# Kernel optimization log

Measured on AMD Instinct MI355X. Metric: run time of the kernel, lower is better.

## Reference

```python
import jax, jax.numpy as jnp
import numpy as np

N = 50000
E = 400000
IN_C, HID, OUT2, NCLS = 128, 512, 64, 2
NEG_SLOPE = 0.2


def setup_inputs() -> dict:
    key = jax.random.key(0)
    ks = jax.random.split(key, 12)
    x = jax.random.normal(ks[0], (N, IN_C), dtype=jnp.float32)
    edge_index = jax.random.randint(ks[1], (2, E), 0, N, dtype=jnp.int64)
    def glorot(k, shape):
        fan_in = shape[0]
        return jax.random.normal(k, shape, dtype=jnp.float32) / np.float32(np.sqrt(fan_in))
    return {
        "x": x,
        "edge_index": edge_index,
        "W1": glorot(ks[2], (IN_C, HID)),
        "a1_src": glorot(ks[3], (HID,)),
        "a1_dst": glorot(ks[4], (HID,)),
        "b1": jnp.zeros((HID,), jnp.float32),
        "W2": glorot(ks[5], (HID, OUT2)),
        "a2_src": glorot(ks[6], (OUT2,)),
        "a2_dst": glorot(ks[7], (OUT2,)),
        "b2": jnp.zeros((OUT2,), jnp.float32),
        "fcW": glorot(ks[8], (OUT2, NCLS)),
        "fcb": jnp.zeros((NCLS,), jnp.float32),
    }


def _gat_conv(h_in, src, dst, W, a_src, a_dst, b):
    # single-head GATConv (PyG defaults: heads=1, negative_slope=0.2, self-loops already added)
    h = h_in @ W                                   # [N, D]
    alpha_s = h @ a_src                            # [N]
    alpha_d = h @ a_dst                            # [N]
    e = jax.nn.leaky_relu(alpha_s[src] + alpha_d[dst], NEG_SLOPE)  # [E']
    # segment softmax over incoming edges of each dst node
    m = jax.ops.segment_max(e, dst, num_segments=N)
    ex = jnp.exp(e - m[dst])
    denom = jax.ops.segment_sum(ex, dst, num_segments=N)
    alpha = ex / denom[dst]                        # [E']
    out = jax.ops.segment_sum(alpha[:, None] * h[src], dst, num_segments=N)
    return out + b


def reference(x, edge_index, W1, a1_src, a1_dst, b1, W2, a2_src, a2_dst, b2, fcW, fcb):
    loops = jnp.arange(N, dtype=edge_index.dtype)
    src = jnp.concatenate([edge_index[0], loops])  # add self loops (PyG default)
    dst = jnp.concatenate([edge_index[1], loops])
    h = jax.nn.relu(_gat_conv(x, src, dst, W1, a1_src, a1_dst, b1))
    h = jax.nn.relu(_gat_conv(h, src, dst, W2, a2_src, a2_dst, b2))
    # F.dropout(training=self.training): identity in eval mode
    return h @ fcW + fcb
```

## Files before the change

kernel.cpp:

```cpp
#include <hip/hip_runtime.h>

#define N_NODES 50000
#define N_EDGES 400000
#define E_TOT   (N_EDGES + N_NODES)
#define IN_C 128
#define HID  512
#define OUT2 64
#define NEG_SLOPE 0.2f

typedef short bf16x8 __attribute__((ext_vector_type(8)));
typedef float f32x4  __attribute__((ext_vector_type(4)));

__device__ __forceinline__ float wave_sum(float v) {
#pragma unroll
  for (int o = 32; o > 0; o >>= 1) v += __shfl_xor(v, o, 64);
  return v;
}
__device__ __forceinline__ int wave_sum_i(int v) {
#pragma unroll
  for (int o = 32; o > 0; o >>= 1) v += __shfl_xor(v, o, 64);
  return v;
}
__device__ __forceinline__ float wave_max(float v) {
#pragma unroll
  for (int o = 32; o > 0; o >>= 1) v = fmaxf(v, __shfl_xor(v, o, 64));
  return v;
}
__device__ __forceinline__ float leaky(float t) {
  return (t > 0.f) ? t : NEG_SLOPE * t;
}

__device__ __forceinline__ unsigned short bf16_rne(float x) {
  unsigned u = __float_as_uint(x);
  u += 0x7fffu + ((u >> 16) & 1u);
  return (unsigned short)(u >> 16);
}
__device__ __forceinline__ void split_bf16(float x, unsigned short& h, unsigned short& l) {
  h = bf16_rne(x);
  float hf = __uint_as_float(((unsigned)h) << 16);
  l = bf16_rne(x - hf);
}

__device__ __forceinline__ int esrc(const int* __restrict__ ei, int e) {
  return (e < N_EDGES) ? ei[e] : (e - N_EDGES);
}
__device__ __forceinline__ int edst(const int* __restrict__ ei, int e) {
  return (e < N_EDGES) ? ei[N_EDGES + e] : (e - N_EDGES);
}

__global__ void count_deg(const int* __restrict__ ei, int* __restrict__ deg) {
  int e = blockIdx.x * blockDim.x + threadIdx.x;
  if (e >= E_TOT) return;
  atomicAdd(&deg[edst(ei, e)], 1);
}

__global__ void scanA(const int* __restrict__ deg, int* __restrict__ bsum) {
  __shared__ int ws[16];
  int t = threadIdx.x, lane = t & 63, w = t >> 6;
  int i = blockIdx.x * 1024 + t;
  int v = (i < N_NODES) ? deg[i] : 0;
  int s = wave_sum_i(v);
  if (lane == 0) ws[w] = s;
  __syncthreads();
  if (t == 0) {
    int tot = 0;
#pragma unroll
    for (int k = 0; k < 16; k++) tot += ws[k];
    bsum[blockIdx.x] = tot;
  }
}

__global__ void scanB(const int* __restrict__ bsum, int* __restrict__ boff, int nb) {
  int lane = threadIdx.x;
  int v = (lane < nb) ? bsum[lane] : 0;
  int sc = v;
#pragma unroll
  for (int off = 1; off < 64; off <<= 1) {
    int u = __shfl_up(sc, off, 64);
    if (lane >= off) sc += u;
  }
  if (lane < nb) boff[lane] = sc - v;
}

__global__ void scanC(const int* __restrict__ deg, const int* __restrict__ boff,
                      int* __restrict__ row_ptr) {
  __shared__ int ws[16];
  int t = threadIdx.x, lane = t & 63, w = t >> 6;
  int i = blockIdx.x * 1024 + t;
  int v = (i < N_NODES) ? deg[i] : 0;
  int sc = v;
#pragma unroll
  for (int off = 1; off < 64; off <<= 1) {
    int u = __shfl_up(sc, off, 64);
    if (lane >= off) sc += u;
  }
  if (lane == 63) ws[w] = sc;
  __syncthreads();
  if (w == 0 && lane < 16) {
    int u = ws[lane];
#pragma unroll
    for (int off = 1; off < 16; off <<= 1) {
      int uu = __shfl_up(u, off, 64);
      if (lane >= off) u += uu;
    }
    ws[lane] = u;
  }
  __syncthreads();
  int excl = ((w > 0) ? ws[w - 1] : 0) + boff[blockIdx.x];
  if (i < N_NODES) row_ptr[i + 1] = sc + excl;
  if (blockIdx.x == 0 && t == 0) row_ptr[0] = 0;
}

__global__ void fill_csr(const int* __restrict__ ei, const int* __restrict__ row_ptr,
                         int* __restrict__ cursor, int* __restrict__ csr_src) {
  int e = blockIdx.x * blockDim.x + threadIdx.x;
  if (e >= E_TOT) return;
  int d = edst(ei, e);
  int pos = atomicAdd(&cursor[d], 1);
  csr_src[row_ptr[d] + pos] = esrc(ei, e);
}

__global__ void prep_w1_frag(const float* __restrict__ W1, unsigned short* __restrict__ W1F) {
  int t = blockIdx.x * 256 + threadIdx.x;
  if (t >= 128 * 64) return;
  int fi = t >> 6, l = t & 63;
  int ks = fi & 3, n = (fi >> 2) & 3, jt = fi >> 4;
  int col = jt * 64 + n * 16 + (l & 15);
  int k0 = ks * 32 + (l >> 4) * 8;
  unsigned short hv[8], lv[8];
#pragma unroll
  for (int e = 0; e < 8; e++)
    split_bf16(W1[(size_t)(k0 + e) * HID + col], hv[e], lv[e]);
  unsigned short* ph = W1F + ((size_t)(fi * 2 + 0) * 64 + l) * 8;
  unsigned short* pl = W1F + ((size_t)(fi * 2 + 1) * 64 + l) * 8;
#pragma unroll
  for (int e = 0; e < 8; e++) { ph[e] = hv[e]; pl[e] = lv[e]; }
}

__global__ void prep_w2_frag(const float* __restrict__ W2, unsigned short* __restrict__ W2F) {
  int t = blockIdx.x * 256 + threadIdx.x;
  if (t >= 64 * 64) return;
  int fi = t >> 6, l = t & 63;
  int n = fi & 3, ks = (fi >> 2) & 1, jt = fi >> 3;
  int col = n * 16 + (l & 15);
  int k0 = jt * 64 + ks * 32 + (l >> 4) * 8;
  unsigned short hv[8], lv[8];
#pragma unroll
  for (int e = 0; e < 8; e++)
    split_bf16(W2[(size_t)(k0 + e) * OUT2 + col], hv[e], lv[e]);
  unsigned short* ph = W2F + ((size_t)(fi * 2 + 0) * 64 + l) * 8;
  unsigned short* pl = W2F + ((size_t)(fi * 2 + 1) * 64 + l) * 8;
#pragma unroll
  for (int e = 0; e < 8; e++) { ph[e] = hv[e]; pl[e] = lv[e]; }
}

__global__ void matvec_w1(const float* __restrict__ W1, const float* __restrict__ a1s,
                          const float* __restrict__ a1d, float* __restrict__ w1s,
                          float* __restrict__ w1d) {
  int wid = (blockIdx.x * blockDim.x + threadIdx.x) >> 6;
  int lane = threadIdx.x & 63;
  if (wid >= IN_C) return;
  const float* row = W1 + (size_t)wid * HID;
  float s = 0.f, d = 0.f;
#pragma unroll
  for (int j0 = 0; j0 < HID; j0 += 64) {
    float w = row[j0 + lane];
    s += w * a1s[j0 + lane];
    d += w * a1d[j0 + lane];
  }
  s = wave_sum(s); d = wave_sum(d);
  if (lane == 0) { w1s[wid] = s; w1d[wid] = d; }
}

__global__ void node_scores128(const float* __restrict__ x, const float* __restrict__ ws,
                               const float* __restrict__ wd, float* __restrict__ as_,
                               float* __restrict__ ad_) {
  int wid = (blockIdx.x * blockDim.x + threadIdx.x) >> 6;
  int lane = threadIdx.x & 63;
  if (wid >= N_NODES) return;
  float2 v = ((const float2*)(x + (size_t)wid * IN_C))[lane];
  float2 w1 = ((const float2*)ws)[lane];
  float2 w2 = ((const float2*)wd)[lane];
  float s = wave_sum(v.x * w1.x + v.y * w1.y);
  float d = wave_sum(v.x * w2.x + v.y * w2.y);
  if (lane == 0) { as_[wid] = s; ad_[wid] = d; }
}

__global__ void sm_agg1(const int* __restrict__ row_ptr, const int* __restrict__ csr_src,
                        const float* __restrict__ as_, const float* __restrict__ ad_,
                        const float* __restrict__ x, float* __restrict__ xa) {
  int wid = (blockIdx.x * blockDim.x + threadIdx.x) >> 6;
  int lane = threadIdx.x & 63;
  if (wid >= N_NODES) return;
  int beg = row_ptr[wid], end = row_ptr[wid + 1];
  int deg = end - beg;
  float adv = ad_[wid];
  float2 acc = make_float2(0.f, 0.f);
  if (deg <= 64) {
    int s = 0; float sc = -3.4e38f;
    if (lane < deg) { s = csr_src[beg + lane]; sc = leaky(as_[s] + adv); }
    float m = wave_max(sc);
    float ex = (lane < deg) ? __expf(sc - m) : 0.f;
    float sum = wave_sum(ex);
    float a = ex / sum;
    for (int kk = 0; kk < deg; kk++) {
      float w = __shfl(a, kk, 64);
      int sv = __shfl(s, kk, 64);
      float2 r = ((const float2*)(x + (size_t)sv * IN_C))[lane];
      acc.x += w * r.x; acc.y += w * r.y;
    }
  } else {
    float m = -3.4e38f;
    for (int k = beg + lane; k < end; k += 64)
      m = fmaxf(m, leaky(as_[csr_src[k]] + adv));
    m = wave_max(m);
    float sum = 0.f;
    for (int k = beg + lane; k < end; k += 64)
      sum += __expf(leaky(as_[csr_src[k]] + adv) - m);
    sum = wave_sum(sum);
    float inv = 1.f / sum;
    for (int k = beg; k < end; k++) {
      int sv = csr_src[k];
      float w = __expf(leaky(as_[sv] + adv) - m) * inv;
      float2 r = ((const float2*)(x + (size_t)sv * IN_C))[lane];
      acc.x += w * r.x; acc.y += w * r.y;
    }
  }
  ((float2*)(xa + (size_t)wid * IN_C))[lane] = acc;
}

__launch_bounds__(256, 2)
__global__ void fused_gemm_mfma(const float* __restrict__ xa,
                                const unsigned short* __restrict__ W1F,
                                const float* __restrict__ b1,
                                const unsigned short* __restrict__ W2F,
                                const float* __restrict__ a2s, const float* __restrict__ a2d,
                                float* __restrict__ h2, float* __restrict__ as2,
                                float* __restrict__ ad2) {
  __shared__ unsigned short Ah[64][128];
  __shared__ unsigned short Al[64][128];
  __shared__ unsigned int   TS[64][64];
  int m0 = blockIdx.x * 64;
  int t = threadIdx.x;
  int w = t >> 6;
  int l = t & 63;
  int lr = l & 15;
  int G  = l >> 4;

#pragma unroll
  for (int j = 0; j < 8; j++) {
    int idx = t + j * 256;
    int row = idx >> 5, c4 = idx & 31;
    int gr = m0 + row;
    float4 v = make_float4(0.f, 0.f, 0.f, 0.f);
    if (gr < N_NODES) v = *(const float4*)(xa + (size_t)gr * IN_C + c4 * 4);
    int k0 = (c4 * 4) ^ ((row & 7) << 3);
    unsigned short h0, l0, h1, l1, h2_, l2_, h3, l3;
    split_bf16(v.x, h0, l0); split_bf16(v.y, h1, l1);
    split_bf16(v.z, h2_, l2_); split_bf16(v.w, h3, l3);
    *(uint2*)&Ah[row][k0] = make_uint2((unsigned)h0 | ((unsigned)h1 << 16),
                                       (unsigned)h2_ | ((unsigned)h3 << 16));
    *(uint2*)&Al[row][k0] = make_uint2((unsigned)l0 | ((unsigned)l1 << 16),
                                       (unsigned)l2_ | ((unsigned)l3 << 16));
  }
  __syncthreads();

  int rowA = w * 16 + lr;
  int swA = (rowA & 7) << 3;
  int sw2 = (rowA & 7) << 2;

  bf16x8 aFh[4], aFl[4];
#pragma unroll
  for (int ks = 0; ks < 4; ks++) {
    int kb = (ks * 32 + G * 8) ^ swA;
    aFh[ks] = *(const bf16x8*)&Ah[rowA][kb];
    aFl[ks] = *(const bf16x8*)&Al[rowA][kb];
  }

  const bf16x8* W1Fv = (const bf16x8*)W1F;
  const bf16x8* W2Fv = (const bf16x8*)W2F;

  f32x4 acc2[4];
#pragma unroll
  for (int n = 0; n < 4; n++) acc2[n] = (f32x4){0.f, 0.f, 0.f, 0.f};

  for (int jt = 0; jt < 8; jt++) {
    f32x4 acc1[4];
#pragma unroll
    for (int n = 0; n < 4; n++) acc1[n] = (f32x4){0.f, 0.f, 0.f, 0.f};
#pragma unroll
    for (int ks = 0; ks < 4; ks++) {
#pragma unroll
      for (int n = 0; n < 4; n++) {
        int fi = (jt * 4 + n) * 4 + ks;
        bf16x8 b_h = W1Fv[(size_t)(fi * 2 + 0) * 64 + l];
        bf16x8 b_l = W1Fv[(size_t)(fi * 2 + 1) * 64 + l];
        acc1[n] = __builtin_amdgcn_mfma_f32_16x16x32_bf16(aFh[ks], b_h, acc1[n], 0, 0, 0);
        acc1[n] = __builtin_amdgcn_mfma_f32_16x16x32_bf16(aFl[ks], b_h, acc1[n], 0, 0, 0);
        acc1[n] = __builtin_amdgcn_mfma_f32_16x16x32_bf16(aFh[ks], b_l, acc1[n], 0, 0, 0);
      }
    }
    __syncthreads();
#pragma unroll
    for (int n = 0; n < 4; n++) {
      float bv = b1[jt * 64 + n * 16 + lr];
#pragma unroll
      for (int r = 0; r < 4; r++) {
        float vv = fmaxf(acc1[n][r] + bv, 0.f);
        unsigned short hh, ll;
        split_bf16(vv, hh, ll);
        int rowL = w * 16 + G * 4 + r;
        int colS = (n * 16 + lr) ^ ((rowL & 7) << 2);
        TS[rowL][colS] = (unsigned)hh | ((unsigned)ll << 16);
      }
    }
    __syncthreads();
#pragma unroll
    for (int ks = 0; ks < 2; ks++) {
      int kl = ks * 32 + G * 8;
      uint4 q0 = *(const uint4*)&TS[rowA][(kl + 0) ^ sw2];
      uint4 q1 = *(const uint4*)&TS[rowA][(kl + 4) ^ sw2];
      bf16x8 a2h, a2l;
      a2h[0] = (short)(q0.x & 0xffff); a2l[0] = (short)(q0.x >> 16);
      a2h[1] = (short)(q0.y & 0xffff); a2l[1] = (short)(q0.y >> 16);
      a2h[2] = (short)(q0.z & 0xffff); a2l[2] = (short)(q0.z >> 16);
      a2h[3] = (short)(q0.w & 0xffff); a2l[3] = (short)(q0.w >> 16);
      a2h[4] = (short)(q1.x & 0xffff); a2l[4] = (short)(q1.x >> 16);
      a2h[5] = (short)(q1.y & 0xffff); a2l[5] = (short)(q1.y >> 16);
      a2h[6] = (short)(q1.z & 0xffff); a2l[6] = (short)(q1.z >> 16);
      a2h[7] = (short)(q1.w & 0xffff); a2l[7] = (short)(q1.w >> 16);
#pragma unroll
      for (int n = 0; n < 4; n++) {
        int fi2 = (jt * 2 + ks) * 4 + n;
        bf16x8 b_h = W2Fv[(size_t)(fi2 * 2 + 0) * 64 + l];
        bf16x8 b_l = W2Fv[(size_t)(fi2 * 2 + 1) * 64 + l];
        acc2[n] = __builtin_amdgcn_mfma_f32_16x16x32_bf16(a2h, b_h, acc2[n], 0, 0, 0);
        acc2[n] = __builtin_amdgcn_mfma_f32_16x16x32_bf16(a2l, b_h, acc2[n], 0, 0, 0);
        acc2[n] = __builtin_amdgcn_mfma_f32_16x16x32_bf16(a2h, b_l, acc2[n], 0, 0, 0);
      }
    }
  }

#pragma unroll
  for (int r = 0; r < 4; r++) {
    int grow = m0 + w * 16 + G * 4 + r;
    if (grow < N_NODES) {
#pragma unroll
      for (int n = 0; n < 4; n++)
        h2[(size_t)grow * OUT2 + n * 16 + lr] = acc2[n][r];
    }
    float sp = 0.f, dp = 0.f;
#pragma unroll
    for (int n = 0; n < 4; n++) {
      float v = acc2[n][r];
      sp += v * a2s[n * 16 + lr];
      dp += v * a2d[n * 16 + lr];
    }
#pragma unroll
    for (int o = 1; o < 16; o <<= 1) {
      sp += __shfl_xor(sp, o, 64);
      dp += __shfl_xor(dp, o, 64);
    }
    if (lr == 0 && grow < N_NODES) { as2[grow] = sp; ad2[grow] = dp; }
  }
}

__global__ void sm_agg2_final(const int* __restrict__ row_ptr, const int* __restrict__ csr_src,
                              const float* __restrict__ as_, const float* __restrict__ ad_,
                              const float* __restrict__ h2, const float* __restrict__ b2,
                              const float* __restrict__ fcW, const float* __restrict__ fcb,
                              float* __restrict__ out) {
  int wid = (blockIdx.x * blockDim.x + threadIdx.x) >> 6;
  int lane = threadIdx.x & 63;
  if (wid >= N_NODES) return;
  int beg = row_ptr[wid], end = row_ptr[wid + 1];
  int deg = end - beg;
  float adv = ad_[wid];
  float acc = 0.f;
  if (deg <= 64) {
    int s = 0; float sc = -3.4e38f;
    if (lane < deg) { s = csr_src[beg + lane]; sc = leaky(as_[s] + adv); }
    float m = wave_max(sc);
    float ex = (lane < deg) ? __expf(sc - m) : 0.f;
    float sum = wave_sum(ex);
    float a = ex / sum;
    for (int kk = 0; kk < deg; kk++) {
      float w = __shfl(a, kk, 64);
      int sv = __shfl(s, kk, 64);
      acc += w * h2[(size_t)sv * OUT2 + lane];
    }
  } else {
    float m = -3.4e38f;
    for (int k = beg + lane; k < end; k += 64)
      m = fmaxf(m, leaky(as_[csr_src[k]] + adv));
    m = wave_max(m);
    float sum = 0.f;
    for (int k = beg + lane; k < end; k += 64)
      sum += __expf(leaky(as_[csr_src[k]] + adv) - m);
    sum = wave_sum(sum);
    float inv = 1.f / sum;
    for (int k = beg; k < end; k++) {
      int sv = csr_src[k];
      float w = __expf(leaky(as_[sv] + adv) - m) * inv;
      acc += w * h2[(size_t)sv * OUT2 + lane];
    }
  }
  float v = fmaxf(acc + b2[lane], 0.f);
  float2 fw = ((const float2*)fcW)[lane];
  float f0 = wave_sum(v * fw.x);
  float f1 = wave_sum(v * fw.y);
  if (lane == 0) {
    out[(size_t)wid * 2 + 0] = f0 + fcb[0];
    out[(size_t)wid * 2 + 1] = f1 + fcb[1];
  }
}

extern "C" void kernel_launch(void* const* d_in, const int* in_sizes, int n_in,
                              void* d_out, int out_size, void* d_ws, size_t ws_size,
                              hipStream_t stream) {
  const float* x    = (const float*)d_in[0];
  const int*   ei   = (const int*)d_in[1];
  const float* W1   = (const float*)d_in[2];
  const float* a1s  = (const float*)d_in[3];
  const float* a1d  = (const float*)d_in[4];
  const float* b1   = (const float*)d_in[5];
  const float* W2   = (const float*)d_in[6];
  const float* a2s  = (const float*)d_in[7];
  const float* a2d  = (const float*)d_in[8];
  const float* b2   = (const float*)d_in[9];
  const float* fcW  = (const float*)d_in[10];
  const float* fcb  = (const float*)d_in[11];
  float* out = (float*)d_out;

  char* p = (char*)d_ws;
  float* xa    = (float*)p; p += (size_t)N_NODES * IN_C * 4;
  float* h2    = (float*)p; p += (size_t)N_NODES * OUT2 * 4;
  float* as1   = (float*)p; p += (size_t)N_NODES * 4;
  float* ad1   = (float*)p; p += (size_t)N_NODES * 4;
  float* w1s   = (float*)p; p += 256 * 4;
  float* w1d   = (float*)p; p += 256 * 4;
  int* row_ptr = (int*)p;   p += (size_t)(N_NODES + 4) * 4;
  int* deg     = (int*)p;   p += (size_t)N_NODES * 4;
  int* bsum    = (int*)p;   p += 64 * 4;
  int* boff    = (int*)p;   p += 64 * 4;
  int* csr_src = (int*)p;   p += (size_t)E_TOT * 4;
  unsigned short* W1F = (unsigned short*)p; p += (size_t)128 * 2 * 64 * 8 * 2;
  unsigned short* W2F = (unsigned short*)p; p += (size_t)64 * 2 * 64 * 8 * 2;

  const int edge_blocks = (E_TOT + 255) / 256;
  const int node_wave_blocks = (N_NODES + 3) / 4;
  const int m_tiles = (N_NODES + 63) / 64;
  const int scan_blocks = (N_NODES + 1023) / 1024;

  hipMemsetAsync(deg, 0, (size_t)N_NODES * 4, stream);
  count_deg<<<edge_blocks, 256, 0, stream>>>(ei, deg);
  scanA<<<scan_blocks, 1024, 0, stream>>>(deg, bsum);
  scanB<<<1, 64, 0, stream>>>(bsum, boff, scan_blocks);
  scanC<<<scan_blocks, 1024, 0, stream>>>(deg, boff, row_ptr);
  hipMemsetAsync(deg, 0, (size_t)N_NODES * 4, stream);
  fill_csr<<<edge_blocks, 256, 0, stream>>>(ei, row_ptr, deg, csr_src);
  prep_w1_frag<<<(128 * 64 + 255) / 256, 256, 0, stream>>>(W1, W1F);
  prep_w2_frag<<<(64 * 64 + 255) / 256, 256, 0, stream>>>(W2, W2F);

  matvec_w1<<<(IN_C + 3) / 4, 256, 0, stream>>>(W1, a1s, a1d, w1s, w1d);
  node_scores128<<<node_wave_blocks, 256, 0, stream>>>(x, w1s, w1d, as1, ad1);
  sm_agg1<<<node_wave_blocks, 256, 0, stream>>>(row_ptr, csr_src, as1, ad1, x, xa);

  fused_gemm_mfma<<<m_tiles, 256, 0, stream>>>(xa, W1F, b1, W2F,
                                               a2s, a2d, h2, as1, ad1);

  sm_agg2_final<<<node_wave_blocks, 256, 0, stream>>>(row_ptr, csr_src, as1, ad1, h2, b2,
                                                      fcW, fcb, out);
}
```

Baseline: 308.3 us.

## Give each GEMM wave two row tiles and unroll gather loops by four

The fused MFMA kernel now runs two waves per block, and each wave owns 32 rows (two 16-row M tiles). Each W1/W2 fragment loaded from global memory is therefore reused across twice as many MFMAs. A-fragments are loaded straight from global memory into registers, which removes the Ah/Al shared staging and the block barriers, since each wave only touches its own rows of TS. Both softmax-aggregation kernels unroll the neighbour gather loop by four so several row loads are in flight at once. The cost is higher register pressure in the GEMM and fewer waves per block.

```diff
diff --git a/kernel.cpp b/kernel.cpp
--- a/kernel.cpp
+++ b/kernel.cpp
@@ -195,6 +195,7 @@
   int beg = row_ptr[wid], end = row_ptr[wid + 1];
   int deg = end - beg;
   float adv = ad_[wid];
+  const float2* x2 = (const float2*)x;
   float2 acc = make_float2(0.f, 0.f);
   if (deg <= 64) {
     int s = 0; float sc = -3.4e38f;
@@ -203,10 +204,23 @@
     float ex = (lane < deg) ? __expf(sc - m) : 0.f;
     float sum = wave_sum(ex);
     float a = ex / sum;
-    for (int kk = 0; kk < deg; kk++) {
+    int kk = 0;
+    for (; kk + 4 <= deg; kk += 4) {
+      float w0 = __shfl(a, kk, 64),     w1 = __shfl(a, kk + 1, 64);
+      float w2 = __shfl(a, kk + 2, 64), w3 = __shfl(a, kk + 3, 64);
+      int s0 = __shfl(s, kk, 64),     s1 = __shfl(s, kk + 1, 64);
+      int s2 = __shfl(s, kk + 2, 64), s3 = __shfl(s, kk + 3, 64);
+      float2 r0 = x2[(size_t)s0 * 64 + lane];
+      float2 r1 = x2[(size_t)s1 * 64 + lane];
+      float2 r2 = x2[(size_t)s2 * 64 + lane];
+      float2 r3 = x2[(size_t)s3 * 64 + lane];
+      acc.x += w0 * r0.x + w1 * r1.x + w2 * r2.x + w3 * r3.x;
+      acc.y += w0 * r0.y + w1 * r1.y + w2 * r2.y + w3 * r3.y;
+    }
+    for (; kk < deg; kk++) {
       float w = __shfl(a, kk, 64);
       int sv = __shfl(s, kk, 64);
-      float2 r = ((const float2*)(x + (size_t)sv * IN_C))[lane];
+      float2 r = x2[(size_t)sv * 64 + lane];
       acc.x += w * r.x; acc.y += w * r.y;
     }
   } else {
@@ -222,14 +236,14 @@
     for (int k = beg; k < end; k++) {
       int sv = csr_src[k];
       float w = __expf(leaky(as_[sv] + adv) - m) * inv;
-      float2 r = ((const float2*)(x + (size_t)sv * IN_C))[lane];
+      float2 r = x2[(size_t)sv * 64 + lane];
       acc.x += w * r.x; acc.y += w * r.y;
     }
   }
   ((float2*)(xa + (size_t)wid * IN_C))[lane] = acc;
 }
 
-__launch_bounds__(256, 2)
+__launch_bounds__(128, 2)
 __global__ void fused_gemm_mfma(const float* __restrict__ xa,
                                 const unsigned short* __restrict__ W1F,
                                 const float* __restrict__ b1,
@@ -237,57 +251,54 @@
                                 const float* __restrict__ a2s, const float* __restrict__ a2d,
                                 float* __restrict__ h2, float* __restrict__ as2,
                                 float* __restrict__ ad2) {
-  __shared__ unsigned short Ah[64][128];
-  __shared__ unsigned short Al[64][128];
-  __shared__ unsigned int   TS[64][64];
-  int m0 = blockIdx.x * 64;
+  __shared__ unsigned int TS[64][64];
   int t = threadIdx.x;
   int w = t >> 6;
   int l = t & 63;
   int lr = l & 15;
   int G  = l >> 4;
-
-#pragma unroll
-  for (int j = 0; j < 8; j++) {
-    int idx = t + j * 256;
-    int row = idx >> 5, c4 = idx & 31;
-    int gr = m0 + row;
-    float4 v = make_float4(0.f, 0.f, 0.f, 0.f);
-    if (gr < N_NODES) v = *(const float4*)(xa + (size_t)gr * IN_C + c4 * 4);
-    int k0 = (c4 * 4) ^ ((row & 7) << 3);
-    unsigned short h0, l0, h1, l1, h2_, l2_, h3, l3;
-    split_bf16(v.x, h0, l0); split_bf16(v.y, h1, l1);
-    split_bf16(v.z, h2_, l2_); split_bf16(v.w, h3, l3);
-    *(uint2*)&Ah[row][k0] = make_uint2((unsigned)h0 | ((unsigned)h1 << 16),
-                                       (unsigned)h2_ | ((unsigned)h3 << 16));
-    *(uint2*)&Al[row][k0] = make_uint2((unsigned)l0 | ((unsigned)l1 << 16),
-                                       (unsigned)l2_ | ((unsigned)l3 << 16));
-  }
-  __syncthreads();
-
-  int rowA = w * 16 + lr;
-  int swA = (rowA & 7) << 3;
-  int sw2 = (rowA & 7) << 2;
-
-  bf16x8 aFh[4], aFl[4];
-#pragma unroll
-  for (int ks = 0; ks < 4; ks++) {
-    int kb = (ks * 32 + G * 8) ^ swA;
-    aFh[ks] = *(const bf16x8*)&Ah[rowA][kb];
-    aFl[ks] = *(const bf16x8*)&Al[rowA][kb];
+  int base = blockIdx.x * 64 + w * 32;
+
+  bf16x8 aFh[2][4], aFl[2][4];
+#pragma unroll
+  for (int m = 0; m < 2; m++) {
+    int grow = base + m * 16 + lr;
+    bool ok = (grow < N_NODES);
+    const float* rp = xa + (size_t)grow * IN_C;
+#pragma unroll
+    for (int ks = 0; ks < 4; ks++) {
+      float4 v0 = make_float4(0.f, 0.f, 0.f, 0.f), v1 = v0;
+      if (ok) {
+        v0 = *(const float4*)(rp + ks * 32 + G * 8);
+        v1 = *(const float4*)(rp + ks * 32 + G * 8 + 4);
+      }
+      unsigned short h, lo;
+      split_bf16(v0.x, h, lo); aFh[m][ks][0] = (short)h; aFl[m][ks][0] = (short)lo;
+      split_bf16(v0.y, h, lo); aFh[m][ks][1] = (short)h; aFl[m][ks][1] = (short)lo;
+      split_bf16(v0.z, h, lo); aFh[m][ks][2] = (short)h; aFl[m][ks][2] = (short)lo;
+      split_bf16(v0.w, h, lo); aFh[m][ks][3] = (short)h; aFl[m][ks][3] = (short)lo;
+      split_bf16(v1.x, h, lo); aFh[m][ks][4] = (short)h; aFl[m][ks][4] = (short)lo;
+      split_bf16(v1.y, h, lo); aFh[m][ks][5] = (short)h; aFl[m][ks][5] = (short)lo;
+      split_bf16(v1.z, h, lo); aFh[m][ks][6] = (short)h; aFl[m][ks][6] = (short)lo;
+      split_bf16(v1.w, h, lo); aFh[m][ks][7] = (short)h; aFl[m][ks][7] = (short)lo;
+    }
   }
 
   const bf16x8* W1Fv = (const bf16x8*)W1F;
   const bf16x8* W2Fv = (const bf16x8*)W2F;
 
-  f32x4 acc2[4];
-#pragma unroll
-  for (int n = 0; n < 4; n++) acc2[n] = (f32x4){0.f, 0.f, 0.f, 0.f};
+  f32x4 acc2[2][4];
+#pragma unroll
+  for (int m = 0; m < 2; m++)
+#pragma unroll
+    for (int n = 0; n < 4; n++) acc2[m][n] = (f32x4){0.f, 0.f, 0.f, 0.f};
 
   for (int jt = 0; jt < 8; jt++) {
-    f32x4 acc1[4];
-#pragma unroll
-    for (int n = 0; n < 4; n++) acc1[n] = (f32x4){0.f, 0.f, 0.f, 0.f};
+    f32x4 acc1[2][4];
+#pragma unroll
+    for (int m = 0; m < 2; m++)
+#pragma unroll
+      for (int n = 0; n < 4; n++) acc1[m][n] = (f32x4){0.f, 0.f, 0.f, 0.f};
 #pragma unroll
     for (int ks = 0; ks < 4; ks++) {
 #pragma unroll
@@ -295,73 +306,88 @@
         int fi = (jt * 4 + n) * 4 + ks;
         bf16x8 b_h = W1Fv[(size_t)(fi * 2 + 0) * 64 + l];
         bf16x8 b_l = W1Fv[(size_t)(fi * 2 + 1) * 64 + l];
-        acc1[n] = __builtin_amdgcn_mfma_f32_16x16x32_bf16(aFh[ks], b_h, acc1[n], 0, 0, 0);
-        acc1[n] = __builtin_amdgcn_mfma_f32_16x16x32_bf16(aFl[ks], b_h, acc1[n], 0, 0, 0);
-        acc1[n] = __builtin_amdgcn_mfma_f32_16x16x32_bf16(aFh[ks], b_l, acc1[n], 0, 0, 0);
-      }
-    }
-    __syncthreads();
+#pragma unroll
+        for (int m = 0; m < 2; m++) {
+          acc1[m][n] = __builtin_amdgcn_mfma_f32_16x16x32_bf16(aFh[m][ks], b_h, acc1[m][n], 0, 0, 0);
+          acc1[m][n] = __builtin_amdgcn_mfma_f32_16x16x32_bf16(aFl[m][ks], b_h, acc1[m][n], 0, 0, 0);
+          acc1[m][n] = __builtin_amdgcn_mfma_f32_16x16x32_bf16(aFh[m][ks], b_l, acc1[m][n], 0, 0, 0);
+        }
+      }
+    }
 #pragma unroll
     for (int n = 0; n < 4; n++) {
       float bv = b1[jt * 64 + n * 16 + lr];
 #pragma unroll
-      for (int r = 0; r < 4; r++) {
-        float vv = fmaxf(acc1[n][r] + bv, 0.f);
-        unsigned short hh, ll;
-        split_bf16(vv, hh, ll);
-        int rowL = w * 16 + G * 4 + r;
-        int colS = (n * 16 + lr) ^ ((rowL & 7) << 2);
-        TS[rowL][colS] = (unsigned)hh | ((unsigned)ll << 16);
-      }
-    }
-    __syncthreads();
+      for (int m = 0; m < 2; m++) {
+#pragma unroll
+        for (int r = 0; r < 4; r++) {
+          float vv = fmaxf(acc1[m][n][r] + bv, 0.f);
+          unsigned short hh, ll;
+          split_bf16(vv, hh, ll);
+          int rowL = w * 32 + m * 16 + G * 4 + r;
+          int colS = (n * 16 + lr) ^ ((rowL & 7) << 2);
+          TS[rowL][colS] = (unsigned)hh | ((unsigned)ll << 16);
+        }
+      }
+    }
 #pragma unroll
     for (int ks = 0; ks < 2; ks++) {
       int kl = ks * 32 + G * 8;
-      uint4 q0 = *(const uint4*)&TS[rowA][(kl + 0) ^ sw2];
-      uint4 q1 = *(const uint4*)&TS[rowA][(kl + 4) ^ sw2];
-      bf16x8 a2h, a2l;
-      a2h[0] = (short)(q0.x & 0xffff); a2l[0] = (short)(q0.x >> 16);
-      a2h[1] = (short)(q0.y & 0xffff); a2l[1] = (short)(q0.y >> 16);
-      a2h[2] = (short)(q0.z & 0xffff); a2l[2] = (short)(q0.z >> 16);
-      a2h[3] = (short)(q0.w & 0xffff); a2l[3] = (short)(q0.w >> 16);
-      a2h[4] = (short)(q1.x & 0xffff); a2l[4] = (short)(q1.x >> 16);
-      a2h[5] = (short)(q1.y & 0xffff); a2l[5] = (short)(q1.y >> 16);
-      a2h[6] = (short)(q1.z & 0xffff); a2l[6] = (short)(q1.z >> 16);
-      a2h[7] = (short)(q1.w & 0xffff); a2l[7] = (short)(q1.w >> 16);
+      bf16x8 a2h[2], a2l[2];
+#pragma unroll
+      for (int m = 0; m < 2; m++) {
+        int rowA = w * 32 + m * 16 + lr;
+        int sw2 = (rowA & 7) << 2;
+        uint4 q0 = *(const uint4*)&TS[rowA][(kl + 0) ^ sw2];
+        uint4 q1 = *(const uint4*)&TS[rowA][(kl + 4) ^ sw2];
+        a2h[m][0] = (short)(q0.x & 0xffff); a2l[m][0] = (short)(q0.x >> 16);
+        a2h[m][1] = (short)(q0.y & 0xffff); a2l[m][1] = (short)(q0.y >> 16);
+        a2h[m][2] = (short)(q0.z & 0xffff); a2l[m][2] = (short)(q0.z >> 16);
+        a2h[m][3] = (short)(q0.w & 0xffff); a2l[m][3] = (short)(q0.w >> 16);
+        a2h[m][4] = (short)(q1.x & 0xffff); a2l[m][4] = (short)(q1.x >> 16);
+        a2h[m][5] = (short)(q1.y & 0xffff); a2l[m][5] = (short)(q1.y >> 16);
+        a2h[m][6] = (short)(q1.z & 0xffff); a2l[m][6] = (short)(q1.z >> 16);
+        a2h[m][7] = (short)(q1.w & 0xffff); a2l[m][7] = (short)(q1.w >> 16);
+      }
 #pragma unroll
       for (int n = 0; n < 4; n++) {
         int fi2 = (jt * 2 + ks) * 4 + n;
         bf16x8 b_h = W2Fv[(size_t)(fi2 * 2 + 0) * 64 + l];
         bf16x8 b_l = W2Fv[(size_t)(fi2 * 2 + 1) * 64 + l];
-        acc2[n] = __builtin_amdgcn_mfma_f32_16x16x32_bf16(a2h, b_h, acc2[n], 0, 0, 0);
-        acc2[n] = __builtin_amdgcn_mfma_f32_16x16x32_bf16(a2l, b_h, acc2[n], 0, 0, 0);
-        acc2[n] = __builtin_amdgcn_mfma_f32_16x16x32_bf16(a2h, b_l, acc2[n], 0, 0, 0);
-      }
-    }
-  }
-
-#pragma unroll
-  for (int r = 0; r < 4; r++) {
-    int grow = m0 + w * 16 + G * 4 + r;
-    if (grow < N_NODES) {
-#pragma unroll
-      for (int n = 0; n < 4; n++)
-        h2[(size_t)grow * OUT2 + n * 16 + lr] = acc2[n][r];
-    }
-    float sp = 0.f, dp = 0.f;
-#pragma unroll
-    for (int n = 0; n < 4; n++) {
-      float v = acc2[n][r];
-      sp += v * a2s[n * 16 + lr];
-      dp += v * a2d[n * 16 + lr];
-    }
-#pragma unroll
-    for (int o = 1; o < 16; o <<= 1) {
-      sp += __shfl_xor(sp, o, 64);
-      dp += __shfl_xor(dp, o, 64);
-    }
-    if (lr == 0 && grow < N_NODES) { as2[grow] = sp; ad2[grow] = dp; }
+#pragma unroll
+        for (int m = 0; m < 2; m++) {
+          acc2[m][n] = __builtin_amdgcn_mfma_f32_16x16x32_bf16(a2h[m], b_h, acc2[m][n], 0, 0, 0);
+          acc2[m][n] = __builtin_amdgcn_mfma_f32_16x16x32_bf16(a2l[m], b_h, acc2[m][n], 0, 0, 0);
+          acc2[m][n] = __builtin_amdgcn_mfma_f32_16x16x32_bf16(a2h[m], b_l, acc2[m][n], 0, 0, 0);
+        }
+      }
+    }
+  }
+
+#pragma unroll
+  for (int m = 0; m < 2; m++) {
+#pragma unroll
+    for (int r = 0; r < 4; r++) {
+      int grow = base + m * 16 + G * 4 + r;
+      if (grow < N_NODES) {
+#pragma unroll
+        for (int n = 0; n < 4; n++)
+          h2[(size_t)grow * OUT2 + n * 16 + lr] = acc2[m][n][r];
+      }
+      float sp = 0.f, dp = 0.f;
+#pragma unroll
+      for (int n = 0; n < 4; n++) {
+        float v = acc2[m][n][r];
+        sp += v * a2s[n * 16 + lr];
+        dp += v * a2d[n * 16 + lr];
+      }
+#pragma unroll
+      for (int o = 1; o < 16; o <<= 1) {
+        sp += __shfl_xor(sp, o, 64);
+        dp += __shfl_xor(dp, o, 64);
+      }
+      if (lr == 0 && grow < N_NODES) { as2[grow] = sp; ad2[grow] = dp; }
+    }
   }
 }
 
@@ -384,7 +410,19 @@
     float ex = (lane < deg) ? __expf(sc - m) : 0.f;
     float sum = wave_sum(ex);
     float a = ex / sum;
-    for (int kk = 0; kk < deg; kk++) {
+    int kk = 0;
+    for (; kk + 4 <= deg; kk += 4) {
+      float w0 = __shfl(a, kk, 64),     w1 = __shfl(a, kk + 1, 64);
+      float w2 = __shfl(a, kk + 2, 64), w3 = __shfl(a, kk + 3, 64);
+      int s0 = __shfl(s, kk, 64),     s1 = __shfl(s, kk + 1, 64);
+      int s2 = __shfl(s, kk + 2, 64), s3 = __shfl(s, kk + 3, 64);
+      float r0 = h2[(size_t)s0 * OUT2 + lane];
+      float r1 = h2[(size_t)s1 * OUT2 + lane];
+      float r2 = h2[(size_t)s2 * OUT2 + lane];
+      float r3 = h2[(size_t)s3 * OUT2 + lane];
+      acc += w0 * r0 + w1 * r1 + w2 * r2 + w3 * r3;
+    }
+    for (; kk < deg; kk++) {
       float w = __shfl(a, kk, 64);
       int sv = __shfl(s, kk, 64);
       acc += w * h2[(size_t)sv * OUT2 + lane];
@@ -449,7 +487,7 @@
 
   const int edge_blocks = (E_TOT + 255) / 256;
   const int node_wave_blocks = (N_NODES + 3) / 4;
-  const int m_tiles = (N_NODES + 63) / 64;
+  const int m_tiles64 = (N_NODES + 63) / 64;
   const int scan_blocks = (N_NODES + 1023) / 1024;
 
   hipMemsetAsync(deg, 0, (size_t)N_NODES * 4, stream);
@@ -466,8 +504,8 @@
   node_scores128<<<node_wave_blocks, 256, 0, stream>>>(x, w1s, w1d, as1, ad1);
   sm_agg1<<<node_wave_blocks, 256, 0, stream>>>(row_ptr, csr_src, as1, ad1, x, xa);
 
-  fused_gemm_mfma<<<m_tiles, 256, 0, stream>>>(xa, W1F, b1, W2F,
-                                               a2s, a2d, h2, as1, ad1);
+  fused_gemm_mfma<<<m_tiles64, 128, 0, stream>>>(xa, W1F, b1, W2F,
+                                                 a2s, a2d, h2, as1, ad1);
 
   sm_agg2_final<<<node_wave_blocks, 256, 0, stream>>>(row_ptr, csr_src, as1, ad1, h2, b2,
                                                       fcW, fcb, out);
```

After: 272.9 us. -11.5%, faster.
